# Kernel tuning notes

Measured on AMD Instinct MI355X. Metric: run time of the kernel, lower is better.

The kernel has to match this reference:

```python
import jax, jax.numpy as jnp
import numpy as np

N_SRC, N_DST, N_EDGE, D_IN, D_HID, D_OUT = 100000, 25000, 300000, 256, 256, 256


def setup_inputs() -> dict:
    key = jax.random.key(0)
    ks = jax.random.split(key, 9)
    # forward tensor args
    h_src = jax.random.normal(ks[0], (N_SRC, D_IN), dtype=jnp.float32)
    h_dst = jax.random.normal(ks[1], (N_DST, D_IN), dtype=jnp.float32)
    weights = jax.random.uniform(ks[2], (N_EDGE,), dtype=jnp.float32)
    src_idx = jax.random.randint(ks[3], (N_EDGE,), 0, N_SRC)
    dst_idx = jax.random.randint(ks[4], (N_EDGE,), 0, N_DST)
    # learned parameters (xavier_uniform with relu gain, zero bias)
    gain = float(np.sqrt(2.0))
    def xavier(k, fan_in, fan_out):
        a = gain * np.sqrt(6.0 / (fan_in + fan_out))
        return jax.random.uniform(k, (fan_in, fan_out), dtype=jnp.float32, minval=-a, maxval=a)
    Q_w = xavier(ks[5], D_IN, D_HID)            # stored [in, out]
    Q_b = jnp.zeros((D_HID,), dtype=jnp.float32)
    W_w = xavier(ks[6], D_IN + D_HID, D_OUT)    # stored [in, out]
    W_b = jnp.zeros((D_OUT,), dtype=jnp.float32)
    return {"h_src": h_src, "h_dst": h_dst, "weights": weights,
            "Q_w": Q_w, "Q_b": Q_b, "W_w": W_w, "W_b": W_b,
            "src_idx": src_idx, "dst_idx": dst_idx}


def reference(h_src, h_dst, weights, Q_w, Q_b, W_w, W_b, src_idx, dst_idx):
    n_dst = h_dst.shape[0]
    # nft = relu(Q(h_src))  (dropout is eval-mode identity)
    nft = jax.nn.relu(h_src @ Q_w + Q_b)                     # [N_src, H]
    # weighted neighbor sum: u_mul_e + sum over edges per dst node
    msg = nft[src_idx] * weights[:, None]                    # [E, H]
    n = jax.ops.segment_sum(msg, dst_idx, num_segments=n_dst)          # [N_dst, H]
    ws = jax.ops.segment_sum(weights, dst_idx, num_segments=n_dst)     # [N_dst]
    ws = jnp.clip(ws, 1.0, None)[:, None]
    z = jax.nn.relu(jnp.concatenate([n / ws, h_dst], axis=1) @ W_w + W_b)  # [N_dst, O]
    z_norm = jnp.linalg.norm(z, ord=2, axis=1, keepdims=True)
    z_norm = jnp.where(z_norm == 0, jnp.float32(1.0), z_norm)
    return z / z_norm
```

## Files before the change

### kernel.cpp

```cpp
#include <hip/hip_runtime.h>
#include <hip/hip_bf16.h>
#include <cstdint>

#define N_SRC 100000
#define N_DST 25000
#define N_EDGE 300000

typedef float f32x4 __attribute__((ext_vector_type(4)));
typedef __bf16 bf16x8 __attribute__((ext_vector_type(8)));

typedef const __attribute__((address_space(1))) void gv_t;
typedef __attribute__((address_space(3))) void lv_t;

__device__ __forceinline__ unsigned short f2bf(float f) {
    union { float f; unsigned int u; } v; v.f = f;
    unsigned int u = v.u;
    u += 0x7FFFu + ((u >> 16) & 1u);
    return (unsigned short)(u >> 16);
}
__device__ __forceinline__ float bf2f(unsigned int bits16) {
    union { unsigned int u; float f; } v; v.u = bits16 << 16;
    return v.f;
}

__global__ void cast_weights(const float* __restrict__ Qw, const float* __restrict__ Ww,
                             unsigned short* __restrict__ Qt, unsigned short* __restrict__ Wt) {
    int i = blockIdx.x * blockDim.x + threadIdx.x;
    if (i < 256 * 256) {
        int n = i >> 8, k = i & 255;
        Qt[n * 256 + k] = f2bf(Qw[k * 256 + n]);
    } else if (i < 256 * 256 + 512 * 256) {
        int j = i - 256 * 256;
        int n = j >> 9, k = j & 511;
        Wt[n * 512 + k] = f2bf(Ww[k * 256 + n]);
    }
}

__global__ void hist_kernel(const int* __restrict__ dst_idx, int* __restrict__ counts) {
    int i = blockIdx.x * blockDim.x + threadIdx.x;
    if (i < N_EDGE) atomicAdd(&counts[dst_idx[i]], 1);
}

__global__ __launch_bounds__(1024) void scan_kernel(const int* __restrict__ counts,
                                                    int* __restrict__ offsets, int n) {
    __shared__ int wsum[16];
    const int t = threadIdx.x;
    const int wid = t >> 6, lane = t & 63;
    int carry = 0;
    if (t == 0) offsets[0] = 0;
    for (int base = 0; base < n; base += 1024) {
        int x = (base + t < n) ? counts[base + t] : 0;
        #pragma unroll
        for (int off = 1; off < 64; off <<= 1) {
            int y = __shfl_up(x, off, 64);
            if (lane >= off) x += y;
        }
        if (lane == 63) wsum[wid] = x;
        __syncthreads();
        if (t < 16) {
            int w = wsum[t];
            #pragma unroll
            for (int off = 1; off < 16; off <<= 1) {
                int y = __shfl_up(w, off, 64);
                if (t >= off) w += y;
            }
            wsum[t] = w;
        }
        __syncthreads();
        int pre = (wid > 0) ? wsum[wid - 1] : 0;
        int incl = carry + pre + x;
        if (base + t < n) offsets[base + t + 1] = incl;
        carry += wsum[15];
        __syncthreads();
    }
}

__global__ void scatter_kernel(const int* __restrict__ dst_idx, const int* __restrict__ offsets,
                               int* __restrict__ counts, int* __restrict__ edge_list) {
    int i = blockIdx.x * blockDim.x + threadIdx.x;
    if (i < N_EDGE) {
        int d = dst_idx[i];
        int pos = offsets[d] + (atomicSub(&counts[d], 1) - 1);
        edge_list[pos] = i;
    }
}

__global__ __launch_bounds__(256) void gemm1_97(
    const float* __restrict__ Af, const unsigned short* __restrict__ Bt,
    const float* __restrict__ bias, unsigned short* __restrict__ Cb)
{
    __shared__ __align__(16) float Asf[2][64 * 64];
    const int tid = threadIdx.x;
    const int wv = tid >> 6, lane = tid & 63, g = lane >> 4, cl = lane & 15;
    const int m0 = blockIdx.x * 64;
    const int n0 = wv * 64;
    const int srow = tid >> 4, sblk = tid & 15;

    f32x4 acc[4][4];
    #pragma unroll
    for (int i = 0; i < 4; ++i)
        #pragma unroll
        for (int j = 0; j < 4; ++j)
            acc[i][j] = (f32x4){0.f, 0.f, 0.f, 0.f};

    auto stage = [&](int buf, int kt) {
        #pragma unroll
        for (int i = 0; i < 4; ++i) {
            const int row = i * 16 + srow;
            const int grow = min(m0 + row, N_SRC - 1);
            const float* gp = Af + (size_t)grow * 256 + kt * 64 + ((sblk ^ (row & 7)) << 2);
            __builtin_amdgcn_global_load_lds(
                (gv_t*)gp,
                (lv_t*)((char*)&Asf[buf][0] + i * 4096 + wv * 1024), 16, 0, 0);
        }
    };

    stage(0, 0);
    __syncthreads();

    #pragma unroll
    for (int kt = 0; kt < 4; ++kt) {
        const int buf = kt & 1;
        if (kt < 3) stage(buf ^ 1, kt + 1);

        uint4 bfrag[2][4];
        #pragma unroll
        for (int ks = 0; ks < 2; ++ks)
            #pragma unroll
            for (int ni = 0; ni < 4; ++ni)
                bfrag[ks][ni] = *reinterpret_cast<const uint4*>(
                    Bt + (size_t)(n0 + ni * 16 + cl) * 256 + kt * 64 + ks * 32 + g * 8);

        #pragma unroll
        for (int ks = 0; ks < 2; ++ks) {
            #pragma unroll
            for (int mi = 0; mi < 4; ++mi) {
                const int row = mi * 16 + cl;
                const f32x4 lo = *reinterpret_cast<const f32x4*>(
                    (const char*)&Asf[buf][0] + row * 256 + (((ks * 8 + g * 2 + 0) ^ (cl & 7)) << 4));
                const f32x4 hi = *reinterpret_cast<const f32x4*>(
                    (const char*)&Asf[buf][0] + row * 256 + (((ks * 8 + g * 2 + 1) ^ (cl & 7)) << 4));
                bf16x8 af;
                af[0] = (__bf16)lo[0]; af[1] = (__bf16)lo[1]; af[2] = (__bf16)lo[2]; af[3] = (__bf16)lo[3];
                af[4] = (__bf16)hi[0]; af[5] = (__bf16)hi[1]; af[6] = (__bf16)hi[2]; af[7] = (__bf16)hi[3];
                #pragma unroll
                for (int ni = 0; ni < 4; ++ni)
                    acc[mi][ni] = __builtin_amdgcn_mfma_f32_16x16x32_bf16(
                        af, __builtin_bit_cast(bf16x8, bfrag[ks][ni]), acc[mi][ni], 0, 0, 0);
            }
        }
        __syncthreads();
    }

    float bcol[4];
    #pragma unroll
    for (int ni = 0; ni < 4; ++ni) bcol[ni] = bias[n0 + ni * 16 + cl];
    #pragma unroll
    for (int mi = 0; mi < 4; ++mi) {
        const int rowb = m0 + mi * 16 + g * 4;
        #pragma unroll
        for (int ni = 0; ni < 4; ++ni) {
            const int col = n0 + ni * 16 + cl;
            #pragma unroll
            for (int r = 0; r < 4; ++r) {
                const int row = rowb + r;
                if (row < N_SRC) {
                    float v = fmaxf(acc[mi][ni][r] + bcol[ni], 0.f);
                    Cb[(size_t)row * 256 + col] = f2bf(v);
                }
            }
        }
    }
}

__global__ __launch_bounds__(256) void gemm2_97(
    const unsigned short* __restrict__ Ab, const unsigned short* __restrict__ Bt,
    const float* __restrict__ bias, float* __restrict__ Cf, int M)
{
    __shared__ __align__(16) unsigned short Ash[2][64 * 64];
    __shared__ float norml[4][64];
    const int tid = threadIdx.x;
    const int wv = tid >> 6, lane = tid & 63, g = lane >> 4, cl = lane & 15;
    const int m0 = blockIdx.x * 64;
    const int n0 = wv * 64;
    const int srow = tid >> 3, sblk = tid & 7;

    f32x4 acc[4][4];
    #pragma unroll
    for (int i = 0; i < 4; ++i)
        #pragma unroll
        for (int j = 0; j < 4; ++j)
            acc[i][j] = (f32x4){0.f, 0.f, 0.f, 0.f};

    auto stage = [&](int buf, int kt) {
        #pragma unroll
        for (int i = 0; i < 2; ++i) {
            const int row = i * 32 + srow;
            const int grow = min(m0 + row, M - 1);
            const unsigned short* gp = Ab + (size_t)grow * 512 + kt * 64 + ((sblk ^ (row & 7)) << 3);
            __builtin_amdgcn_global_load_lds(
                (gv_t*)gp,
                (lv_t*)((char*)&Ash[buf][0] + i * 4096 + wv * 1024), 16, 0, 0);
        }
    };

    stage(0, 0);
    __syncthreads();

    #pragma unroll
    for (int kt = 0; kt < 8; ++kt) {
        const int buf = kt & 1;
        if (kt < 7) stage(buf ^ 1, kt + 1);

        uint4 bfrag[2][4];
        #pragma unroll
        for (int ks = 0; ks < 2; ++ks)
            #pragma unroll
            for (int ni = 0; ni < 4; ++ni)
                bfrag[ks][ni] = *reinterpret_cast<const uint4*>(
                    Bt + (size_t)(n0 + ni * 16 + cl) * 512 + kt * 64 + ks * 32 + g * 8);

        #pragma unroll
        for (int ks = 0; ks < 2; ++ks) {
            #pragma unroll
            for (int mi = 0; mi < 4; ++mi) {
                const int row = mi * 16 + cl;
                const bf16x8 af = *reinterpret_cast<const bf16x8*>(
                    (const char*)&Ash[buf][0] + row * 128 + (((ks * 4 + g) ^ (cl & 7)) << 4));
                #pragma unroll
                for (int ni = 0; ni < 4; ++ni)
                    acc[mi][ni] = __builtin_amdgcn_mfma_f32_16x16x32_bf16(
                        af, __builtin_bit_cast(bf16x8, bfrag[ks][ni]), acc[mi][ni], 0, 0, 0);
            }
        }
        __syncthreads();
    }

    float bcol[4];
    #pragma unroll
    for (int ni = 0; ni < 4; ++ni) bcol[ni] = bias[n0 + ni * 16 + cl];

    #pragma unroll
    for (int mi = 0; mi < 4; ++mi) {
        #pragma unroll
        for (int r = 0; r < 4; ++r) {
            float s = 0.f;
            #pragma unroll
            for (int ni = 0; ni < 4; ++ni) {
                float v = fmaxf(acc[mi][ni][r] + bcol[ni], 0.f);
                acc[mi][ni][r] = v;
                s += v * v;
            }
            #pragma unroll
            for (int m = 1; m < 16; m <<= 1) s += __shfl_xor(s, m, 64);
            if (cl == 0) norml[wv][mi * 16 + g * 4 + r] = s;
        }
    }
    __syncthreads();
    #pragma unroll
    for (int mi = 0; mi < 4; ++mi) {
        #pragma unroll
        for (int r = 0; r < 4; ++r) {
            const int rl = mi * 16 + g * 4 + r;
            const float tot = norml[0][rl] + norml[1][rl] + norml[2][rl] + norml[3][rl];
            const float rn = tot > 0.f ? rsqrtf(tot) : 1.0f;
            const int row = m0 + rl;
            if (row < M) {
                #pragma unroll
                for (int ni = 0; ni < 4; ++ni)
                    Cf[(size_t)row * 256 + n0 + ni * 16 + cl] = acc[mi][ni][r] * rn;
            }
        }
    }
}

__global__ __launch_bounds__(256) void aggregate_kernel(
    const unsigned short* __restrict__ nft, const float* __restrict__ h_dst,
    const float* __restrict__ weights, const int* __restrict__ src_idx,
    const int* __restrict__ edge_list, const int* __restrict__ offsets,
    unsigned short* __restrict__ xb)
{
    int d = blockIdx.x * 4 + (threadIdx.x >> 6);
    if (d >= N_DST) return;
    int lane = threadIdx.x & 63;
    int p0 = offsets[d], p1 = offsets[d + 1];
    float a0 = 0.f, a1 = 0.f, a2 = 0.f, a3 = 0.f, wsum = 0.f;
    int p = p0;
    for (; p + 1 < p1; p += 2) {
        int e0 = edge_list[p], e1 = edge_list[p + 1];
        float w0 = weights[e0], w1 = weights[e1];
        int s0 = src_idx[e0], s1 = src_idx[e1];
        uint2 v0 = *reinterpret_cast<const uint2*>(nft + (size_t)s0 * 256 + lane * 4);
        uint2 v1 = *reinterpret_cast<const uint2*>(nft + (size_t)s1 * 256 + lane * 4);
        wsum += w0 + w1;
        a0 += w0 * bf2f(v0.x & 0xffffu) + w1 * bf2f(v1.x & 0xffffu);
        a1 += w0 * bf2f(v0.x >> 16)     + w1 * bf2f(v1.x >> 16);
        a2 += w0 * bf2f(v0.y & 0xffffu) + w1 * bf2f(v1.y & 0xffffu);
        a3 += w0 * bf2f(v0.y >> 16)     + w1 * bf2f(v1.y >> 16);
    }
    if (p < p1) {
        int e = edge_list[p];
        float w = weights[e];
        int s = src_idx[e];
        wsum += w;
        uint2 v = *reinterpret_cast<const uint2*>(nft + (size_t)s * 256 + lane * 4);
        a0 += w * bf2f(v.x & 0xffffu);
        a1 += w * bf2f(v.x >> 16);
        a2 += w * bf2f(v.y & 0xffffu);
        a3 += w * bf2f(v.y >> 16);
    }
    float inv = 1.0f / fmaxf(wsum, 1.0f);
    uint2 pk;
    pk.x = (unsigned)f2bf(a0 * inv) | ((unsigned)f2bf(a1 * inv) << 16);
    pk.y = (unsigned)f2bf(a2 * inv) | ((unsigned)f2bf(a3 * inv) << 16);
    *reinterpret_cast<uint2*>(xb + (size_t)d * 512 + lane * 4) = pk;
    float4 h = *reinterpret_cast<const float4*>(h_dst + (size_t)d * 256 + lane * 4);
    uint2 q;
    q.x = (unsigned)f2bf(h.x) | ((unsigned)f2bf(h.y) << 16);
    q.y = (unsigned)f2bf(h.z) | ((unsigned)f2bf(h.w) << 16);
    *reinterpret_cast<uint2*>(xb + (size_t)d * 512 + 256 + lane * 4) = q;
}

extern "C" void kernel_launch(void* const* d_in, const int* in_sizes, int n_in,
                              void* d_out, int out_size, void* d_ws, size_t ws_size,
                              hipStream_t stream) {
    const float* h_src   = (const float*)d_in[0];
    const float* h_dst   = (const float*)d_in[1];
    const float* weights = (const float*)d_in[2];
    const float* Q_w     = (const float*)d_in[3];
    const float* Q_b     = (const float*)d_in[4];
    const float* W_w     = (const float*)d_in[5];
    const float* W_b     = (const float*)d_in[6];
    const int* src_idx   = (const int*)d_in[7];
    const int* dst_idx   = (const int*)d_in[8];
    float* out = (float*)d_out;

    char* ws = (char*)d_ws;
    unsigned short* nft = (unsigned short*)(ws);
    unsigned short* xb  = (unsigned short*)(ws + 51200000);
    unsigned short* Qt  = (unsigned short*)(ws + 76800000);
    unsigned short* Wt  = (unsigned short*)(ws + 76931072);
    int* counts    = (int*)(ws + 77193216);
    int* offsets   = (int*)(ws + 77293216);
    int* edge_list = (int*)(ws + 77393220);

    hipMemsetAsync(counts, 0, N_DST * sizeof(int), stream);

    cast_weights<<<768, 256, 0, stream>>>(Q_w, W_w, Qt, Wt);
    hist_kernel<<<(N_EDGE + 255) / 256, 256, 0, stream>>>(dst_idx, counts);
    scan_kernel<<<1, 1024, 0, stream>>>(counts, offsets, N_DST);
    scatter_kernel<<<(N_EDGE + 255) / 256, 256, 0, stream>>>(dst_idx, offsets, counts, edge_list);

    gemm1_97<<<(N_SRC + 63) / 64, 256, 0, stream>>>(h_src, Qt, Q_b, nft);

    aggregate_kernel<<<N_DST / 4, 256, 0, stream>>>(
        nft, h_dst, weights, src_idx, edge_list, offsets, xb);

    gemm2_97<<<(N_DST + 63) / 64, 256, 0, stream>>>(xb, Wt, W_b, out, N_DST);

    (void)in_sizes; (void)n_in; (void)out_size; (void)ws_size;
}
```

Measured before the change: 191.2 us.

## Load full-K A tile and B fragments into registers once in both GEMMs

Both GEMMs drop the double-buffered K-loop. Each block now stages the entire 64-row A tile in LDS once (gemm1 converts fp32 to bf16 on the way in) and holds the whole K range of B fragments in registers, then runs all MFMAs after a single barrier. This removes the per-K-step barriers and the repeated fp32-to-bf16 conversion in the inner loop. In exchange it uses much more LDS and registers, which lowers occupancy (waves_per_eu 1-2), and loads are no longer overlapped with compute. The aggregate loop is also unrolled from 2 to 4 edges to raise memory-level parallelism.

```diff
diff --git a/kernel.cpp b/kernel.cpp
--- a/kernel.cpp
+++ b/kernel.cpp
@@ -85,71 +85,59 @@
     }
 }
 
-__global__ __launch_bounds__(256) void gemm1_97(
-    const float* __restrict__ Af, const unsigned short* __restrict__ Bt,
-    const float* __restrict__ bias, unsigned short* __restrict__ Cb)
+__global__ __launch_bounds__(256) __attribute__((amdgpu_waves_per_eu(1, 2)))
+void gemm1_v2(const float* __restrict__ Af, const unsigned short* __restrict__ Bt,
+              const float* __restrict__ bias, unsigned short* __restrict__ Cb)
 {
-    __shared__ __align__(16) float Asf[2][64 * 64];
+    __shared__ __align__(16) unsigned char As[32768];
     const int tid = threadIdx.x;
     const int wv = tid >> 6, lane = tid & 63, g = lane >> 4, cl = lane & 15;
     const int m0 = blockIdx.x * 64;
     const int n0 = wv * 64;
-    const int srow = tid >> 4, sblk = tid & 15;
-
-    f32x4 acc[4][4];
-    #pragma unroll
-    for (int i = 0; i < 4; ++i)
-        #pragma unroll
-        for (int j = 0; j < 4; ++j)
-            acc[i][j] = (f32x4){0.f, 0.f, 0.f, 0.f};
-
-    auto stage = [&](int buf, int kt) {
-        #pragma unroll
-        for (int i = 0; i < 4; ++i) {
-            const int row = i * 16 + srow;
-            const int grow = min(m0 + row, N_SRC - 1);
-            const float* gp = Af + (size_t)grow * 256 + kt * 64 + ((sblk ^ (row & 7)) << 2);
-            __builtin_amdgcn_global_load_lds(
-                (gv_t*)gp,
-                (lv_t*)((char*)&Asf[buf][0] + i * 4096 + wv * 1024), 16, 0, 0);
-        }
-    };
-
-    stage(0, 0);
+
+    uint4 Br[4][8];
+    #pragma unroll
+    for (int ni = 0; ni < 4; ++ni)
+        #pragma unroll
+        for (int kf = 0; kf < 8; ++kf)
+            Br[ni][kf] = *reinterpret_cast<const uint4*>(
+                Bt + (size_t)(n0 + ni * 16 + cl) * 256 + kf * 32 + g * 8);
+
+    {
+        const int row = tid >> 2, q = tid & 3;
+        const int grow = min(m0 + row, N_SRC - 1);
+        const float* gp = Af + (size_t)grow * 256 + q * 64;
+        #pragma unroll
+        for (int j = 0; j < 8; ++j) {
+            const float4 lo = *reinterpret_cast<const float4*>(gp + j * 8);
+            const float4 hi = *reinterpret_cast<const float4*>(gp + j * 8 + 4);
+            uint4 pk;
+            pk.x = (unsigned)f2bf(lo.x) | ((unsigned)f2bf(lo.y) << 16);
+            pk.y = (unsigned)f2bf(lo.z) | ((unsigned)f2bf(lo.w) << 16);
+            pk.z = (unsigned)f2bf(hi.x) | ((unsigned)f2bf(hi.y) << 16);
+            pk.w = (unsigned)f2bf(hi.z) | ((unsigned)f2bf(hi.w) << 16);
+            const int c = q * 8 + j;
+            *reinterpret_cast<uint4*>(&As[row * 512 + ((c ^ (row & 7)) << 4)]) = pk;
+        }
+    }
     __syncthreads();
 
-    #pragma unroll
-    for (int kt = 0; kt < 4; ++kt) {
-        const int buf = kt & 1;
-        if (kt < 3) stage(buf ^ 1, kt + 1);
-
-        uint4 bfrag[2][4];
-        #pragma unroll
-        for (int ks = 0; ks < 2; ++ks)
+    f32x4 acc[4][4] = {};
+    #pragma unroll
+    for (int kf = 0; kf < 8; ++kf) {
+        bf16x8 af[4];
+        #pragma unroll
+        for (int mi = 0; mi < 4; ++mi) {
+            const int row = mi * 16 + cl;
+            af[mi] = *reinterpret_cast<const bf16x8*>(
+                &As[row * 512 + (((kf * 4 + g) ^ (cl & 7)) << 4)]);
+        }
+        #pragma unroll
+        for (int mi = 0; mi < 4; ++mi)
             #pragma unroll
             for (int ni = 0; ni < 4; ++ni)
-                bfrag[ks][ni] = *reinterpret_cast<const uint4*>(
-                    Bt + (size_t)(n0 + ni * 16 + cl) * 256 + kt * 64 + ks * 32 + g * 8);
-
-        #pragma unroll
-        for (int ks = 0; ks < 2; ++ks) {
-            #pragma unroll
-            for (int mi = 0; mi < 4; ++mi) {
-                const int row = mi * 16 + cl;
-                const f32x4 lo = *reinterpret_cast<const f32x4*>(
-                    (const char*)&Asf[buf][0] + row * 256 + (((ks * 8 + g * 2 + 0) ^ (cl & 7)) << 4));
-                const f32x4 hi = *reinterpret_cast<const f32x4*>(
-                    (const char*)&Asf[buf][0] + row * 256 + (((ks * 8 + g * 2 + 1) ^ (cl & 7)) << 4));
-                bf16x8 af;
-                af[0] = (__bf16)lo[0]; af[1] = (__bf16)lo[1]; af[2] = (__bf16)lo[2]; af[3] = (__bf16)lo[3];
-                af[4] = (__bf16)hi[0]; af[5] = (__bf16)hi[1]; af[6] = (__bf16)hi[2]; af[7] = (__bf16)hi[3];
-                #pragma unroll
-                for (int ni = 0; ni < 4; ++ni)
-                    acc[mi][ni] = __builtin_amdgcn_mfma_f32_16x16x32_bf16(
-                        af, __builtin_bit_cast(bf16x8, bfrag[ks][ni]), acc[mi][ni], 0, 0, 0);
-            }
-        }
-        __syncthreads();
+                acc[mi][ni] = __builtin_amdgcn_mfma_f32_16x16x32_bf16(
+                    af[mi], __builtin_bit_cast(bf16x8, Br[ni][kf]), acc[mi][ni], 0, 0, 0);
     }
 
     float bcol[4];
@@ -173,73 +161,76 @@
     }
 }
 
-__global__ __launch_bounds__(256) void gemm2_97(
-    const unsigned short* __restrict__ Ab, const unsigned short* __restrict__ Bt,
-    const float* __restrict__ bias, float* __restrict__ Cf, int M)
+__global__ __launch_bounds__(256) __attribute__((amdgpu_waves_per_eu(1, 2)))
+void gemm2_v2(const unsigned short* __restrict__ Ab, const unsigned short* __restrict__ Bt,
+              const float* __restrict__ bias, float* __restrict__ Cf, int M)
 {
-    __shared__ __align__(16) unsigned short Ash[2][64 * 64];
-    __shared__ float norml[4][64];
+    __shared__ __align__(16) unsigned char As[65536];
     const int tid = threadIdx.x;
     const int wv = tid >> 6, lane = tid & 63, g = lane >> 4, cl = lane & 15;
     const int m0 = blockIdx.x * 64;
     const int n0 = wv * 64;
-    const int srow = tid >> 3, sblk = tid & 7;
-
-    f32x4 acc[4][4];
-    #pragma unroll
-    for (int i = 0; i < 4; ++i)
-        #pragma unroll
-        for (int j = 0; j < 4; ++j)
-            acc[i][j] = (f32x4){0.f, 0.f, 0.f, 0.f};
-
-    auto stage = [&](int buf, int kt) {
-        #pragma unroll
-        for (int i = 0; i < 2; ++i) {
-            const int row = i * 32 + srow;
-            const int grow = min(m0 + row, M - 1);
-            const unsigned short* gp = Ab + (size_t)grow * 512 + kt * 64 + ((sblk ^ (row & 7)) << 3);
-            __builtin_amdgcn_global_load_lds(
-                (gv_t*)gp,
-                (lv_t*)((char*)&Ash[buf][0] + i * 4096 + wv * 1024), 16, 0, 0);
-        }
+
+    uint4 Br[4][8];
+    auto loadB = [&](int p) {
+        #pragma unroll
+        for (int ni = 0; ni < 4; ++ni)
+            #pragma unroll
+            for (int kf = 0; kf < 8; ++kf)
+                Br[ni][kf] = *reinterpret_cast<const uint4*>(
+                    Bt + (size_t)(n0 + ni * 16 + cl) * 512 + (p * 8 + kf) * 32 + g * 8);
     };
-
-    stage(0, 0);
+    loadB(0);
+
+    #pragma unroll
+    for (int j = 0; j < 16; ++j) {
+        const int row = wv * 16 + j;
+        const int grow = min(m0 + row, M - 1);
+        const unsigned short* gp = Ab + (size_t)grow * 512 + ((lane ^ (row & 7)) << 3);
+        __builtin_amdgcn_global_load_lds((gv_t*)gp, (lv_t*)&As[row * 1024], 16, 0, 0);
+    }
     __syncthreads();
 
-    #pragma unroll
-    for (int kt = 0; kt < 8; ++kt) {
-        const int buf = kt & 1;
-        if (kt < 7) stage(buf ^ 1, kt + 1);
-
-        uint4 bfrag[2][4];
-        #pragma unroll
-        for (int ks = 0; ks < 2; ++ks)
+    f32x4 acc[4][4] = {};
+    #pragma unroll
+    for (int kf = 0; kf < 8; ++kf) {
+        bf16x8 af[4];
+        #pragma unroll
+        for (int mi = 0; mi < 4; ++mi) {
+            const int row = mi * 16 + cl;
+            af[mi] = *reinterpret_cast<const bf16x8*>(
+                &As[row * 1024 + (((kf * 4 + g) ^ (cl & 7)) << 4)]);
+        }
+        #pragma unroll
+        for (int mi = 0; mi < 4; ++mi)
             #pragma unroll
             for (int ni = 0; ni < 4; ++ni)
-                bfrag[ks][ni] = *reinterpret_cast<const uint4*>(
-                    Bt + (size_t)(n0 + ni * 16 + cl) * 512 + kt * 64 + ks * 32 + g * 8);
-
-        #pragma unroll
-        for (int ks = 0; ks < 2; ++ks) {
-            #pragma unroll
-            for (int mi = 0; mi < 4; ++mi) {
-                const int row = mi * 16 + cl;
-                const bf16x8 af = *reinterpret_cast<const bf16x8*>(
-                    (const char*)&Ash[buf][0] + row * 128 + (((ks * 4 + g) ^ (cl & 7)) << 4));
-                #pragma unroll
-                for (int ni = 0; ni < 4; ++ni)
-                    acc[mi][ni] = __builtin_amdgcn_mfma_f32_16x16x32_bf16(
-                        af, __builtin_bit_cast(bf16x8, bfrag[ks][ni]), acc[mi][ni], 0, 0, 0);
-            }
-        }
-        __syncthreads();
+                acc[mi][ni] = __builtin_amdgcn_mfma_f32_16x16x32_bf16(
+                    af[mi], __builtin_bit_cast(bf16x8, Br[ni][kf]), acc[mi][ni], 0, 0, 0);
+    }
+    loadB(1);
+    #pragma unroll
+    for (int kf = 8; kf < 16; ++kf) {
+        bf16x8 af[4];
+        #pragma unroll
+        for (int mi = 0; mi < 4; ++mi) {
+            const int row = mi * 16 + cl;
+            af[mi] = *reinterpret_cast<const bf16x8*>(
+                &As[row * 1024 + (((kf * 4 + g) ^ (cl & 7)) << 4)]);
+        }
+        #pragma unroll
+        for (int mi = 0; mi < 4; ++mi)
+            #pragma unroll
+            for (int ni = 0; ni < 4; ++ni)
+                acc[mi][ni] = __builtin_amdgcn_mfma_f32_16x16x32_bf16(
+                    af[mi], __builtin_bit_cast(bf16x8, Br[ni][kf - 8]), acc[mi][ni], 0, 0, 0);
     }
 
     float bcol[4];
     #pragma unroll
     for (int ni = 0; ni < 4; ++ni) bcol[ni] = bias[n0 + ni * 16 + cl];
 
+    float ssq[4][4];
     #pragma unroll
     for (int mi = 0; mi < 4; ++mi) {
         #pragma unroll
@@ -253,8 +244,17 @@
             }
             #pragma unroll
             for (int m = 1; m < 16; m <<= 1) s += __shfl_xor(s, m, 64);
-            if (cl == 0) norml[wv][mi * 16 + g * 4 + r] = s;
-        }
+            ssq[mi][r] = s;
+        }
+    }
+    __syncthreads();
+    float* norml = reinterpret_cast<float*>(As);
+    if (cl == 0) {
+        #pragma unroll
+        for (int mi = 0; mi < 4; ++mi)
+            #pragma unroll
+            for (int r = 0; r < 4; ++r)
+                norml[wv * 64 + mi * 16 + g * 4 + r] = ssq[mi][r];
     }
     __syncthreads();
     #pragma unroll
@@ -262,7 +262,7 @@
         #pragma unroll
         for (int r = 0; r < 4; ++r) {
             const int rl = mi * 16 + g * 4 + r;
-            const float tot = norml[0][rl] + norml[1][rl] + norml[2][rl] + norml[3][rl];
+            const float tot = norml[rl] + norml[64 + rl] + norml[128 + rl] + norml[192 + rl];
             const float rn = tot > 0.f ? rsqrtf(tot) : 1.0f;
             const int row = m0 + rl;
             if (row < M) {
@@ -286,19 +286,25 @@
     int p0 = offsets[d], p1 = offsets[d + 1];
     float a0 = 0.f, a1 = 0.f, a2 = 0.f, a3 = 0.f, wsum = 0.f;
     int p = p0;
-    for (; p + 1 < p1; p += 2) {
-        int e0 = edge_list[p], e1 = edge_list[p + 1];
-        float w0 = weights[e0], w1 = weights[e1];
-        int s0 = src_idx[e0], s1 = src_idx[e1];
+    for (; p + 3 < p1; p += 4) {
+        int e0 = edge_list[p], e1 = edge_list[p + 1], e2 = edge_list[p + 2], e3 = edge_list[p + 3];
+        float w0 = weights[e0], w1 = weights[e1], w2 = weights[e2], w3 = weights[e3];
+        int s0 = src_idx[e0], s1 = src_idx[e1], s2 = src_idx[e2], s3 = src_idx[e3];
         uint2 v0 = *reinterpret_cast<const uint2*>(nft + (size_t)s0 * 256 + lane * 4);
         uint2 v1 = *reinterpret_cast<const uint2*>(nft + (size_t)s1 * 256 + lane * 4);
-        wsum += w0 + w1;
-        a0 += w0 * bf2f(v0.x & 0xffffu) + w1 * bf2f(v1.x & 0xffffu);
-        a1 += w0 * bf2f(v0.x >> 16)     + w1 * bf2f(v1.x >> 16);
-        a2 += w0 * bf2f(v0.y & 0xffffu) + w1 * bf2f(v1.y & 0xffffu);
-        a3 += w0 * bf2f(v0.y >> 16)     + w1 * bf2f(v1.y >> 16);
-    }
-    if (p < p1) {
+        uint2 v2 = *reinterpret_cast<const uint2*>(nft + (size_t)s2 * 256 + lane * 4);
+        uint2 v3 = *reinterpret_cast<const uint2*>(nft + (size_t)s3 * 256 + lane * 4);
+        wsum += (w0 + w1) + (w2 + w3);
+        a0 += w0 * bf2f(v0.x & 0xffffu) + w1 * bf2f(v1.x & 0xffffu)
+            + w2 * bf2f(v2.x & 0xffffu) + w3 * bf2f(v3.x & 0xffffu);
+        a1 += w0 * bf2f(v0.x >> 16)     + w1 * bf2f(v1.x >> 16)
+            + w2 * bf2f(v2.x >> 16)     + w3 * bf2f(v3.x >> 16);
+        a2 += w0 * bf2f(v0.y & 0xffffu) + w1 * bf2f(v1.y & 0xffffu)
+            + w2 * bf2f(v2.y & 0xffffu) + w3 * bf2f(v3.y & 0xffffu);
+        a3 += w0 * bf2f(v0.y >> 16)     + w1 * bf2f(v1.y >> 16)
+            + w2 * bf2f(v2.y >> 16)     + w3 * bf2f(v3.y >> 16);
+    }
+    for (; p < p1; ++p) {
         int e = edge_list[p];
         float w = weights[e];
         int s = src_idx[e];
@@ -351,12 +357,12 @@
     scan_kernel<<<1, 1024, 0, stream>>>(counts, offsets, N_DST);
     scatter_kernel<<<(N_EDGE + 255) / 256, 256, 0, stream>>>(dst_idx, offsets, counts, edge_list);
 
-    gemm1_97<<<(N_SRC + 63) / 64, 256, 0, stream>>>(h_src, Qt, Q_b, nft);
+    gemm1_v2<<<(N_SRC + 63) / 64, 256, 0, stream>>>(h_src, Qt, Q_b, nft);
 
     aggregate_kernel<<<N_DST / 4, 256, 0, stream>>>(
         nft, h_dst, weights, src_idx, edge_list, offsets, xb);
 
-    gemm2_97<<<(N_DST + 63) / 64, 256, 0, stream>>>(xb, Wt, W_b, out, N_DST);
+    gemm2_v2<<<(N_DST + 63) / 64, 256, 0, stream>>>(xb, Wt, W_b, out, N_DST);
 
     (void)in_sizes; (void)n_in; (void)out_size; (void)ws_size;
 }
```

Result: slower. 226.0 us (+18.2%).
